# Kernel optimization log

Hardware: AMD Instinct MI355X
Metric: run time of the kernel (lower is better)

Reference implementation:

```python
import jax, jax.numpy as jnp
import numpy as np

P, G, N = 32, 256, 6890  # preds, gallery size, SMPL vertices per person


def _procrustes_v2v(pred, gt):
    """Similarity (Procrustes) align pred->gt, return mean per-vertex L2 error.
    pred, gt: (M, 3) point clouds (M = 2*N, both people jointly aligned)."""
    mu_p = pred.mean(axis=0)
    mu_g = gt.mean(axis=0)
    Xp = pred - mu_p
    Xg = gt - mu_g
    var_p = jnp.sum(Xp * Xp)
    K = Xp.T @ Xg                      # (3,3) cross-covariance
    U, s, Vh = jnp.linalg.svd(K)
    V = Vh.T
    d = jnp.sign(jnp.linalg.det(V @ U.T))  # reflection fix
    D = jnp.stack([jnp.ones_like(d), jnp.ones_like(d), d])
    R = (V * D[None, :]) @ U.T         # rotation, det(R)=+1
    scale = jnp.sum(s * D) / var_p
    aligned = scale * (Xp @ R.T) + mu_g
    return jnp.linalg.norm(aligned - gt, axis=-1).mean()


def setup_inputs() -> dict:
    key = jax.random.key(0)
    k1, k2 = jax.random.split(key)
    pred_vertices = jax.random.normal(k1, (P, 2, N, 3), dtype=jnp.float32)
    target = jax.random.normal(k2, (G, 2, N, 3), dtype=jnp.float32)
    return {"pred_vertices": pred_vertices, "target": target}


def reference(pred_vertices, target):
    # flatten the two-person meshes into a single joint point cloud per sample
    pred = pred_vertices.reshape(pred_vertices.shape[0], -1, 3)  # (P, 2N, 3)
    gt = target.reshape(target.shape[0], -1, 3)                  # (G, 2N, 3)
    # all-pairs procrustes v2v errors: (P, G)
    pair_err = jax.vmap(lambda p: jax.vmap(lambda g: _procrustes_v2v(p, g))(gt))(pred)
    mapping = jnp.argmin(pair_err, axis=1)   # best gt index per prediction
    min_error = jnp.min(pair_err, axis=1)    # its v2v error
    return mapping, min_error
```

## Files before the change

### kernel.cpp

```cpp
#include <hip/hip_runtime.h>
#include <math.h>

#define P_ 32
#define G_ 256
#define NV 6890
#define M_ (2 * NV)
#define QUADS (M_ / 4)
#define NPAIR (P_ * G_)
#define NB_WS 256
#define CHUNK_Q 128
#define NCHUNKS ((QUADS + CHUNK_Q - 1) / CHUNK_Q)

typedef float v2f __attribute__((ext_vector_type(2)));
__device__ inline v2f v2(float a, float b) { v2f r; r.x = a; r.y = b; return r; }
__device__ inline v2f vsplat(float a) { v2f r; r.x = a; r.y = a; return r; }
__device__ inline v2f vfma(v2f a, v2f b, v2f c) { return __builtin_elementwise_fma(a, b, c); }

struct WS {
    float mu_p[P_][3];
    float var_p[P_];
    float mu_g[G_][3];
    float At[NPAIR][12];
    float Kmat[NPAIR][9];
    float pair_err[NPAIR];
};

__device__ inline double block_reduce(double v, double* smem) {
#pragma unroll
    for (int off = 32; off > 0; off >>= 1) v += __shfl_down(v, off, 64);
    int wid  = threadIdx.x >> 6;
    int lane = threadIdx.x & 63;
    __syncthreads();
    if (lane == 0) smem[wid] = v;
    __syncthreads();
    double r = 0.0;
    if (threadIdx.x == 0) {
        int nw = blockDim.x >> 6;
        for (int w = 0; w < nw; ++w) r += smem[w];
    }
    return r;
}

__global__ __launch_bounds__(512) void crosscov_ws(const float* __restrict__ pred,
                                                   const float* __restrict__ gt,
                                                   WS* __restrict__ ws) {
    int bx = blockIdx.x;
    int t = threadIdx.x;

    if (bx >= NB_WS) {
        int b = bx - NB_WS;
        bool isP = (b < P_);
        const float* base = isP ? pred + (size_t)b * (M_ * 3)
                                : gt + (size_t)(b - P_) * (M_ * 3);
        double sx = 0, sy = 0, sz = 0, sq = 0;
        for (int q = t; q < QUADS; q += 512) {
            const float4* p4 = (const float4*)(base + 12 * (size_t)q);
            float4 a = p4[0], c = p4[1], d = p4[2];
            sx += (double)a.x + (double)a.w + (double)c.z + (double)d.y;
            sy += (double)a.y + (double)c.x + (double)c.w + (double)d.z;
            sz += (double)a.z + (double)c.y + (double)d.x + (double)d.w;
            if (isP) {
                sq += (double)a.x * a.x + (double)a.y * a.y + (double)a.z * a.z +
                      (double)a.w * a.w + (double)c.x * c.x + (double)c.y * c.y +
                      (double)c.z * c.z + (double)c.w * c.w + (double)d.x * d.x +
                      (double)d.y * d.y + (double)d.z * d.z + (double)d.w * d.w;
            }
        }
        __shared__ double smem[8];
        double rx = block_reduce(sx, smem);
        double ry = block_reduce(sy, smem);
        double rz = block_reduce(sz, smem);
        double rq = block_reduce(sq, smem);
        if (t == 0) {
            double mx = rx / M_, my = ry / M_, mz = rz / M_;
            if (isP) {
                ws->mu_p[b][0] = (float)mx;
                ws->mu_p[b][1] = (float)my;
                ws->mu_p[b][2] = (float)mz;
                ws->var_p[b] = (float)(rq - (mx * mx + my * my + mz * mz) * (double)M_);
            } else {
                ws->mu_g[b - P_][0] = (float)mx;
                ws->mu_g[b - P_][1] = (float)my;
                ws->mu_g[b - P_][2] = (float)mz;
            }
        }
        return;
    }

    int gbase = (bx & 63) * 4;
    int pbase = (bx >> 6) * 8;
    int wave = t >> 6;
    int lane = t & 63;
    int p = pbase + wave;

    const float* pb = pred + (size_t)p * (M_ * 3);
    int ss = t >> 7;
    int si = t & 127;
    const float4* gsrc = (const float4*)(gt + (size_t)(gbase + ss) * (M_ * 3));

    __shared__ __align__(16) float glds[3][4][CHUNK_Q * 4];

    v2f a01[4], a34[4], a67[4], a25[4];
    float a8[4];
#pragma unroll
    for (int i = 0; i < 4; ++i) {
        a01[i] = vsplat(0.f); a34[i] = vsplat(0.f);
        a67[i] = vsplat(0.f); a25[i] = vsplat(0.f);
        a8[i] = 0.f;
    }

    for (int c = 0; c < NCHUNKS; ++c) {
        int qb = c * CHUNK_Q;
        int nq = QUADS - qb; if (nq > CHUNK_Q) nq = CHUNK_Q;
        __syncthreads();
#pragma unroll
        for (int r = 0; r < 3; ++r) {
            int fi = si + r * 128;
            if (fi < 3 * nq) {
                float4 v = gsrc[(size_t)qb * 3 + fi];
                float vv[4] = { v.x, v.y, v.z, v.w };
#pragma unroll
                for (int j = 0; j < 4; ++j) {
                    int f = 4 * fi + j;
                    glds[f % 3][ss][f / 3] = vv[j];
                }
            }
        }
        __syncthreads();
#pragma unroll
        for (int sub = 0; sub < 2; ++sub) {
            int qq = lane + sub * 64;
            if (qq < nq) {
                const float4* p4 = (const float4*)(pb + 12 * (size_t)(qb + qq));
                float4 Pa = p4[0], Pc = p4[1], Pd = p4[2];
                float x[4] = { Pa.x, Pa.w, Pc.z, Pd.y };
                float y[4] = { Pa.y, Pc.x, Pc.w, Pd.z };
                float z[4] = { Pa.z, Pc.y, Pd.x, Pd.w };
#pragma unroll
                for (int gg = 0; gg < 4; ++gg) {
                    float4 GX = *(const float4*)&glds[0][gg][4 * qq];
                    float4 GY = *(const float4*)&glds[1][gg][4 * qq];
                    float4 GZ = *(const float4*)&glds[2][gg][4 * qq];
                    float gxv[4] = { GX.x, GX.y, GX.z, GX.w };
                    float gyv[4] = { GY.x, GY.y, GY.z, GY.w };
                    float gzv[4] = { GZ.x, GZ.y, GZ.z, GZ.w };
#pragma unroll
                    for (int k = 0; k < 4; ++k) {
                        v2f gxy = v2(gxv[k], gyv[k]);
                        a01[gg] = vfma(vsplat(x[k]), gxy, a01[gg]);
                        a34[gg] = vfma(vsplat(y[k]), gxy, a34[gg]);
                        a67[gg] = vfma(vsplat(z[k]), gxy, a67[gg]);
                        a25[gg] = vfma(v2(x[k], y[k]), vsplat(gzv[k]), a25[gg]);
                        a8[gg]  = fmaf(z[k], gzv[k], a8[gg]);
                    }
                }
            }
        }
    }

    float K[4][9];
#pragma unroll
    for (int i = 0; i < 4; ++i) {
        K[i][0] = a01[i].x; K[i][1] = a01[i].y; K[i][2] = a25[i].x;
        K[i][3] = a34[i].x; K[i][4] = a34[i].y; K[i][5] = a25[i].y;
        K[i][6] = a67[i].x; K[i][7] = a67[i].y; K[i][8] = a8[i];
    }
#pragma unroll
    for (int i = 0; i < 4; ++i)
#pragma unroll
        for (int j = 0; j < 9; ++j) {
            float v = K[i][j];
            v += __shfl_xor(v, 1);  v += __shfl_xor(v, 2);
            v += __shfl_xor(v, 4);  v += __shfl_xor(v, 8);
            v += __shfl_xor(v, 16); v += __shfl_xor(v, 32);
            K[i][j] = v;
        }
    if (lane == 0) {
#pragma unroll
        for (int gg = 0; gg < 4; ++gg)
#pragma unroll
            for (int j = 0; j < 9; ++j)
                ws->Kmat[(gbase + gg) * P_ + p][j] = K[gg][j];
    }
}

__global__ void pair_svd(WS* __restrict__ ws) {
    int pair = blockIdx.x * blockDim.x + threadIdx.x;
    if (pair >= NPAIR) return;
    int p = pair & 31;
    int g = pair >> 5;

    double mp[3] = { ws->mu_p[p][0], ws->mu_p[p][1], ws->mu_p[p][2] };
    double mg[3] = { ws->mu_g[g][0], ws->mu_g[g][1], ws->mu_g[g][2] };
    double varp = (double)ws->var_p[p];

    double K[3][3];
#pragma unroll
    for (int a = 0; a < 3; ++a)
#pragma unroll
        for (int b = 0; b < 3; ++b)
            K[a][b] = (double)ws->Kmat[pair][3 * a + b] - (double)M_ * mp[a] * mg[b];

    double S[3][3];
#pragma unroll
    for (int a = 0; a < 3; ++a)
#pragma unroll
        for (int b = 0; b < 3; ++b) {
            double acc = 0.0;
#pragma unroll
            for (int c = 0; c < 3; ++c) acc += K[c][a] * K[c][b];
            S[a][b] = acc;
        }

    double V[3][3] = { {1, 0, 0}, {0, 1, 0}, {0, 0, 1} };
    double tr = S[0][0] + S[1][1] + S[2][2];
    double tol = 1e-30 * tr * tr + 1e-300;
    const int PP[3] = {0, 0, 1};
    const int QQ[3] = {1, 2, 2};
    for (int sweep = 0; sweep < 30; ++sweep) {
        double off = S[0][1] * S[0][1] + S[0][2] * S[0][2] + S[1][2] * S[1][2];
        if (off <= tol) break;
        for (int r3 = 0; r3 < 3; ++r3) {
            int pq = PP[r3], qq = QQ[r3];
            double apq = S[pq][qq];
            if (apq == 0.0) continue;
            double theta = (S[qq][qq] - S[pq][pq]) / (2.0 * apq);
            double tt = copysign(1.0, theta) / (fabs(theta) + sqrt(theta * theta + 1.0));
            double c = 1.0 / sqrt(tt * tt + 1.0);
            double sj = tt * c;
            for (int r = 0; r < 3; ++r) {
                double srp = S[r][pq], srq = S[r][qq];
                S[r][pq] = c * srp - sj * srq;
                S[r][qq] = sj * srp + c * srq;
            }
            for (int cc = 0; cc < 3; ++cc) {
                double spr = S[pq][cc], sqr = S[qq][cc];
                S[pq][cc] = c * spr - sj * sqr;
                S[qq][cc] = sj * spr + c * sqr;
            }
            for (int r = 0; r < 3; ++r) {
                double vrp = V[r][pq], vrq = V[r][qq];
                V[r][pq] = c * vrp - sj * vrq;
                V[r][qq] = sj * vrp + c * vrq;
            }
        }
    }

    double lam[3] = { S[0][0], S[1][1], S[2][2] };
    int idx[3] = { 0, 1, 2 };
    if (lam[idx[0]] < lam[idx[1]]) { int tt = idx[0]; idx[0] = idx[1]; idx[1] = tt; }
    if (lam[idx[0]] < lam[idx[2]]) { int tt = idx[0]; idx[0] = idx[2]; idx[2] = tt; }
    if (lam[idx[1]] < lam[idx[2]]) { int tt = idx[1]; idx[1] = idx[2]; idx[2] = tt; }
    double Vs[3][3];
    double sv[3];
#pragma unroll
    for (int i = 0; i < 3; ++i) {
        double l = lam[idx[i]];
        sv[i] = sqrt(l > 0.0 ? l : 0.0);
        for (int r = 0; r < 3; ++r) Vs[r][i] = V[r][idx[i]];
    }

    double U[3][3];
#pragma unroll
    for (int i = 0; i < 3; ++i) {
        double kx = K[0][0] * Vs[0][i] + K[0][1] * Vs[1][i] + K[0][2] * Vs[2][i];
        double ky = K[1][0] * Vs[0][i] + K[1][1] * Vs[1][i] + K[1][2] * Vs[2][i];
        double kz = K[2][0] * Vs[0][i] + K[2][1] * Vs[1][i] + K[2][2] * Vs[2][i];
        double inv = (sv[i] > 1e-12 * sv[0] && sv[i] > 0.0) ? 1.0 / sv[i] : 0.0;
        U[0][i] = kx * inv; U[1][i] = ky * inv; U[2][i] = kz * inv;
    }
    if (sv[2] <= 1e-12 * sv[0] || sv[0] == 0.0) {
        U[0][2] = U[1][0] * U[2][1] - U[2][0] * U[1][1];
        U[1][2] = U[2][0] * U[0][1] - U[0][0] * U[2][1];
        U[2][2] = U[0][0] * U[1][1] - U[1][0] * U[0][1];
    }

    double detK = K[0][0] * (K[1][1] * K[2][2] - K[1][2] * K[2][1])
                - K[0][1] * (K[1][0] * K[2][2] - K[1][2] * K[2][0])
                + K[0][2] * (K[1][0] * K[2][1] - K[1][1] * K[2][0]);
    double d = (detK >= 0.0) ? 1.0 : -1.0;
    double scale = (sv[0] + sv[1] + d * sv[2]) / varp;

    float A[9];
#pragma unroll
    for (int a = 0; a < 3; ++a)
#pragma unroll
        for (int b = 0; b < 3; ++b) {
            double r = Vs[a][0] * U[b][0] + Vs[a][1] * U[b][1] + d * Vs[a][2] * U[b][2];
            A[3 * a + b] = (float)(scale * r);
        }
    float tvec[3];
#pragma unroll
    for (int a = 0; a < 3; ++a)
        tvec[a] = (float)(mg[a] - ((double)A[3 * a + 0] * mp[0] + (double)A[3 * a + 1] * mp[1] +
                                   (double)A[3 * a + 2] * mp[2]));

#pragma unroll
    for (int j = 0; j < 9; ++j) ws->At[pair][j] = A[j];
#pragma unroll
    for (int j = 0; j < 3; ++j) ws->At[pair][9 + j] = tvec[j];
}

__global__ __launch_bounds__(256, 3) void pair_error_p(const float* __restrict__ pred,
                                                       const float* __restrict__ gt,
                                                       WS* __restrict__ ws) {
    int bx = blockIdx.x;
    int gbase = (bx & 63) * 4;
    int pbase = (bx >> 6) * 2;
    int t = threadIdx.x;

    v2f a03[8], a14[8], a25v[8], t01[8];
    float a6[8], a7[8], a8v[8], t2[8];
#pragma unroll
    for (int gg = 0; gg < 4; ++gg)
#pragma unroll
        for (int pp = 0; pp < 2; ++pp) {
            int i = gg * 2 + pp;
            const float* At = ws->At[(gbase + gg) * P_ + (pbase + pp)];
            a03[i] = v2(At[0], At[3]);
            a14[i] = v2(At[1], At[4]);
            a25v[i] = v2(At[2], At[5]);
            t01[i] = v2(At[9], At[10]);
            a6[i] = At[6]; a7[i] = At[7]; a8v[i] = At[8]; t2[i] = At[11];
        }

    const float* pb0 = pred + (size_t)pbase * (M_ * 3);
    const float* pb1 = pred + (size_t)(pbase + 1) * (M_ * 3);
    const float* gb[4];
#pragma unroll
    for (int j = 0; j < 4; ++j) gb[j] = gt + (size_t)(gbase + j) * (M_ * 3);

    float acc[8];
#pragma unroll
    for (int i = 0; i < 8; ++i) acc[i] = 0.f;

    for (int q = t; q < QUADS; q += 256) {
        float4 P[2][3];
        {
            const float4* p4 = (const float4*)(pb0 + 12 * (size_t)q);
            P[0][0] = p4[0]; P[0][1] = p4[1]; P[0][2] = p4[2];
            p4 = (const float4*)(pb1 + 12 * (size_t)q);
            P[1][0] = p4[0]; P[1][1] = p4[1]; P[1][2] = p4[2];
        }
#pragma unroll
        for (int gg = 0; gg < 4; ++gg) {
            const float4* g4 = (const float4*)(gb[gg] + 12 * (size_t)q);
            float4 Ga = g4[0], Gc = g4[1], Gd = g4[2];
            v2f gxy[4] = { v2(Ga.x, Ga.y), v2(Ga.w, Gc.x), v2(Gc.z, Gc.w), v2(Gd.y, Gd.z) };
            float gz[4] = { Ga.z, Gc.y, Gd.x, Gd.w };
#pragma unroll
            for (int pp = 0; pp < 2; ++pp) {
                int i = gg * 2 + pp;
                float4 Pa = P[pp][0], Pc = P[pp][1], Pd = P[pp][2];
                float x[4] = { Pa.x, Pa.w, Pc.z, Pd.y };
                float y[4] = { Pa.y, Pc.x, Pc.w, Pd.z };
                float z[4] = { Pa.z, Pc.y, Pd.x, Pd.w };
                float s = 0.f;
#pragma unroll
                for (int k = 0; k < 4; ++k) {
                    v2f dd = vfma(a03[i], vsplat(x[k]),
                             vfma(a14[i], vsplat(y[k]),
                             vfma(a25v[i], vsplat(z[k]), t01[i])));
                    dd = dd - gxy[k];
                    float dz = fmaf(a6[i], x[k], fmaf(a7[i], y[k], fmaf(a8v[i], z[k], t2[i]))) - gz[k];
                    v2f m = dd * dd;
                    s += __builtin_amdgcn_sqrtf(fmaf(dz, dz, m.x + m.y));
                }
                acc[i] += s;
            }
        }
    }

#pragma unroll
    for (int i = 0; i < 8; ++i) {
        float v = acc[i];
        v += __shfl_xor(v, 1);  v += __shfl_xor(v, 2);
        v += __shfl_xor(v, 4);  v += __shfl_xor(v, 8);
        v += __shfl_xor(v, 16); v += __shfl_xor(v, 32);
        acc[i] = v;
    }
    __shared__ float part[4][8];
    int lane = t & 63, wave = t >> 6;
    if (lane == 0) {
#pragma unroll
        for (int i = 0; i < 8; ++i) part[wave][i] = acc[i];
    }
    __syncthreads();
    if (t < 8) {
        float s = part[0][t] + part[1][t] + part[2][t] + part[3][t];
        int gg = t >> 1, pp = t & 1;
        ws->pair_err[(gbase + gg) * P_ + (pbase + pp)] = s / (float)M_;
    }
}

__global__ void argmin_out(const WS* __restrict__ ws, float* __restrict__ out) {
    __shared__ float be[8][32];
    __shared__ int   bg[8][32];
    int t = threadIdx.x;
    int p = t & 31, slice = t >> 5;
    float best = 3.4e38f;
    int bi = G_;
    for (int g = slice; g < G_; g += 8) {
        float e = ws->pair_err[g * P_ + p];
        if (e < best) { best = e; bi = g; }
    }
    be[slice][p] = best;
    bg[slice][p] = bi;
    __syncthreads();
    if (t < P_) {
        float b0 = be[0][t];
        int   i0 = bg[0][t];
        for (int s = 1; s < 8; ++s) {
            float e = be[s][t];
            int   i = bg[s][t];
            if (e < b0 || (e == b0 && i < i0)) { b0 = e; i0 = i; }
        }
        out[t] = (float)i0;
        out[P_ + t] = b0;
    }
}

extern "C" void kernel_launch(void* const* d_in, const int* in_sizes, int n_in,
                              void* d_out, int out_size, void* d_ws, size_t ws_size,
                              hipStream_t stream) {
    const float* pred = (const float*)d_in[0];
    const float* gt   = (const float*)d_in[1];
    float* out = (float*)d_out;
    WS* ws = (WS*)d_ws;

    crosscov_ws<<<dim3(NB_WS + P_ + G_), dim3(512), 0, stream>>>(pred, gt, ws);
    pair_svd<<<dim3(NPAIR / 64), dim3(64), 0, stream>>>(ws);
    pair_error_p<<<dim3(16 * 64), dim3(256), 0, stream>>>(pred, gt, ws);
    argmin_out<<<dim3(1), dim3(256), 0, stream>>>(ws, out);
}
```

Before: 223.5 us.

## Split cross-covariance accumulation over two vertex halves and prefetch gallery chunks

Doubles the number of cross-covariance blocks by splitting the vertex chunk loop into two halves, each writing a partial K matrix that the SVD kernel sums. This gives more blocks to fill the GPU. It also software-prefetches the next gallery chunk into registers while the current chunk is staged into LDS, overlapping global load latency with compute. The cost is extra register pressure, a second K buffer and a few more loads in the SVD stage.

```diff
diff --git a/kernel.cpp b/kernel.cpp
--- a/kernel.cpp
+++ b/kernel.cpp
@@ -7,9 +7,10 @@
 #define M_ (2 * NV)
 #define QUADS (M_ / 4)
 #define NPAIR (P_ * G_)
-#define NB_WS 256
+#define NB_WS 512
 #define CHUNK_Q 128
 #define NCHUNKS ((QUADS + CHUNK_Q - 1) / CHUNK_Q)
+#define HALF_CH 14
 
 typedef float v2f __attribute__((ext_vector_type(2)));
 __device__ inline v2f v2(float a, float b) { v2f r; r.x = a; r.y = b; return r; }
@@ -21,7 +22,7 @@
     float var_p[P_];
     float mu_g[G_][3];
     float At[NPAIR][12];
-    float Kmat[NPAIR][9];
+    float Kmat[2][NPAIR][9];
     float pair_err[NPAIR];
 };
 
@@ -87,8 +88,12 @@
         return;
     }
 
-    int gbase = (bx & 63) * 4;
-    int pbase = (bx >> 6) * 8;
+    int qhalf = bx >> 8;
+    int rem = bx & 255;
+    int gbase = (rem & 63) * 4;
+    int pbase = (rem >> 6) * 8;
+    int c0 = qhalf * HALF_CH;
+    int c1 = qhalf ? NCHUNKS : HALF_CH;
     int wave = t >> 6;
     int lane = t & 63;
     int p = pbase + wave;
@@ -109,7 +114,19 @@
         a8[i] = 0.f;
     }
 
-    for (int c = 0; c < NCHUNKS; ++c) {
+    float4 stg[3];
+    {
+        int qb = c0 * CHUNK_Q;
+        int nq = QUADS - qb; if (nq > CHUNK_Q) nq = CHUNK_Q;
+#pragma unroll
+        for (int r = 0; r < 3; ++r) {
+            int fi = si + r * 128;
+            stg[r] = (fi < 3 * nq) ? gsrc[(size_t)qb * 3 + fi]
+                                   : make_float4(0.f, 0.f, 0.f, 0.f);
+        }
+    }
+
+    for (int c = c0; c < c1; ++c) {
         int qb = c * CHUNK_Q;
         int nq = QUADS - qb; if (nq > CHUNK_Q) nq = CHUNK_Q;
         __syncthreads();
@@ -117,13 +134,21 @@
         for (int r = 0; r < 3; ++r) {
             int fi = si + r * 128;
             if (fi < 3 * nq) {
-                float4 v = gsrc[(size_t)qb * 3 + fi];
-                float vv[4] = { v.x, v.y, v.z, v.w };
+                float vv[4] = { stg[r].x, stg[r].y, stg[r].z, stg[r].w };
 #pragma unroll
                 for (int j = 0; j < 4; ++j) {
                     int f = 4 * fi + j;
                     glds[f % 3][ss][f / 3] = vv[j];
                 }
+            }
+        }
+        if (c + 1 < c1) {
+            int qb2 = (c + 1) * CHUNK_Q;
+            int nq2 = QUADS - qb2; if (nq2 > CHUNK_Q) nq2 = CHUNK_Q;
+#pragma unroll
+            for (int r = 0; r < 3; ++r) {
+                int fi = si + r * 128;
+                if (fi < 3 * nq2) stg[r] = gsrc[(size_t)qb2 * 3 + fi];
             }
         }
         __syncthreads();
@@ -180,7 +205,7 @@
         for (int gg = 0; gg < 4; ++gg)
 #pragma unroll
             for (int j = 0; j < 9; ++j)
-                ws->Kmat[(gbase + gg) * P_ + p][j] = K[gg][j];
+                ws->Kmat[qhalf][(gbase + gg) * P_ + p][j] = K[gg][j];
     }
 }
 
@@ -199,7 +224,9 @@
     for (int a = 0; a < 3; ++a)
 #pragma unroll
         for (int b = 0; b < 3; ++b)
-            K[a][b] = (double)ws->Kmat[pair][3 * a + b] - (double)M_ * mp[a] * mg[b];
+            K[a][b] = (double)ws->Kmat[0][pair][3 * a + b] +
+                      (double)ws->Kmat[1][pair][3 * a + b] -
+                      (double)M_ * mp[a] * mg[b];
 
     double S[3][3];
 #pragma unroll
```

Measured after the change: 216.2 us. 3.2% less time.
